# Performance work log

Hardware: AMD Instinct MI355X
Metric: run time of the kernel (lower is better)

The kernel has to match this reference:

```python
import jax, jax.numpy as jnp
import numpy as np
import math

B, L, D, H = 2, 4096, 1024, 16
DH = D // H


def _build_table(seq_len):
    # Faithful port of build_hierarchical_index_lookup_table (static, host-side).
    assert seq_len & (seq_len - 1) == 0
    levels = int(math.log2(seq_len))
    max_valid = 2 * seq_len - 3
    idx = np.full((seq_len, levels), -1, dtype=np.int64)
    cm = np.zeros((seq_len, levels), dtype=bool)
    for n in range(seq_len):
        c = n
        for lvl in range(levels):
            if lvl == 0:
                nxt = c ^ 1
                pair = c
            else:
                nxt = (c // 2 + seq_len) ^ 1
                pair = c // 2 + seq_len
            if nxt > max_valid:
                break
            if pair < nxt:
                cm[n, lvl] = True
            idx[n, lvl] = nxt
            c = nxt
    return idx, cm


def setup_inputs() -> dict:
    rng = jax.random.key(0)
    ks = jax.random.split(rng, 8)
    s = 0.02  # init scale for weights
    idx, cm = _build_table(L)
    return {
        "query": jax.random.normal(ks[0], (B, L, D), jnp.float32),
        "key": jax.random.normal(ks[1], (B, L, D), jnp.float32),
        "value": jax.random.normal(ks[2], (B, L, D), jnp.float32),
        "Wq": jax.random.normal(ks[3], (D, D), jnp.float32) * s,
        "Wk": jax.random.normal(ks[4], (D, D), jnp.float32) * s,
        "Wv": jax.random.normal(ks[5], (D, D), jnp.float32) * s,
        "Wo": jax.random.normal(ks[6], (D, D), jnp.float32) * s,
        "bo": jax.random.normal(ks[7], (D,), jnp.float32) * s,
        "idx_table": jnp.asarray(idx),        # [L, log2(L)] int64
        "causal_mask": jnp.asarray(cm),       # [L, log2(L)] bool
    }


def reference(query, key, value, Wq, Wk, Wv, Wo, bo, idx_table, causal_mask):
    Bq, Lq, Dm = query.shape
    scale = 1.0 / math.sqrt(DH)

    def heads(x, W):  # nn.Linear (no bias) + split heads -> [B,H,L,Dh]
        return (x @ W.T).reshape(Bq, Lq, H, DH).transpose(0, 2, 1, 3)

    Q = heads(query, Wq)
    K = heads(key, Wk)
    V = heads(value, Wv)

    # Build binary-tree hierarchy. Pair weights come from softmax of ZERO
    # logits (Q_parent starts as zeros in the source), so w0 = w1 = 0.5 exactly.
    Ks, Vs = [K], [V]
    while Ks[-1].shape[2] > 1:
        k, v = Ks[-1], Vs[-1]
        Lc = k.shape[2]
        k2 = k.reshape(Bq, H, Lc // 2, 2, DH)
        v2 = v.reshape(Bq, H, Lc // 2, 2, DH)
        Ks.append(0.5 * (k2[:, :, :, 0] + k2[:, :, :, 1]))
        Vs.append(v2[:, :, :, 0] + v2[:, :, :, 1])
    flatK = jnp.concatenate(Ks, axis=2)  # [B,H,2L-1,Dh]
    flatV = jnp.concatenate(Vs, axis=2)

    # Gather neighbor nodes across levels: [B,H,L,levels,Dh]
    nk = flatK[:, :, idx_table]
    nv = flatV[:, :, idx_table]

    self_logits = jnp.einsum('bhnd,bhnd->bhn', Q, K) * scale
    nbr_logits = jnp.einsum('bhld,bhlnd->bhln', Q, nk) * scale
    nbr_logits = jnp.where(causal_mask[None, None], -jnp.inf, nbr_logits)

    all_logits = jnp.concatenate([self_logits[..., None], nbr_logits], axis=-1)
    w = jax.nn.softmax(all_logits, axis=-1)           # [B,H,L,1+levels]
    all_v = jnp.concatenate([V[:, :, :, None, :], nv], axis=3)
    out = jnp.einsum('bhln,bhlnd->bhld', w, all_v)    # [B,H,L,Dh]
    out = out.transpose(0, 2, 1, 3).reshape(Bq, Lq, Dm)
    return out @ Wo.T + bo
```

## Files before the change

kernel.cpp:

```cpp
#include <hip/hip_runtime.h>
#include <cstdint>
#include <cstddef>


typedef __bf16 bf16;
typedef __bf16 bf16x8 __attribute__((ext_vector_type(8)));
typedef __bf16 bf16x4 __attribute__((ext_vector_type(4)));
typedef float  f32x4  __attribute__((ext_vector_type(4)));

#define L_SEQ  4096
#define NFLAT  8192

__device__ __forceinline__ int off_l(int l) { return 8192 - (8192 >> l); }

__device__ __forceinline__ void glds16(const bf16* g, bf16* l) {
  __builtin_amdgcn_global_load_lds(
      (const __attribute__((address_space(1))) unsigned int*)g,
      (__attribute__((address_space(3))) unsigned int*)l, 16, 0, 0);
}

#define MEMFENCE asm volatile("" ::: "memory")
__device__ __forceinline__ void barrier_raw() {
  MEMFENCE; __builtin_amdgcn_s_barrier(); MEMFENCE;
}

__device__ __forceinline__ int swz(int b) { return b ^ (((b >> 9) & 1) << 5); }
__device__ __forceinline__ int la(int row, int col) {
  return ((((row >> 4) << 1) + (col >> 5)) << 10) + ((row & 15) << 6) + ((col & 31) << 1);
}

__global__ __launch_bounds__(256) void cvtall_kernel(
    const float* __restrict__ q, const float* __restrict__ k, const float* __restrict__ v,
    const float* __restrict__ wq, const float* __restrict__ wk,
    const float* __restrict__ wv, const float* __restrict__ wo,
    bf16* __restrict__ qx, bf16* __restrict__ kx, bf16* __restrict__ vx,
    bf16* __restrict__ wqx, bf16* __restrict__ wkx, bf16* __restrict__ wvx,
    bf16* __restrict__ wox) {
  const int y = blockIdx.y;
  int i = blockIdx.x * 256 + threadIdx.x;
  const float* src; bf16* dst;
  if (y < 3) {
    src = (y == 0) ? q : (y == 1) ? k : v;
    dst = (y == 0) ? qx : (y == 1) ? kx : vx;
  } else {
    if (i >= 1048576) return;
    const int w = i >> 18; i &= 262143;
    src = (w == 0) ? wq : (w == 1) ? wk : (w == 2) ? wv : wo;
    dst = (w == 0) ? wqx : (w == 1) ? wkx : (w == 2) ? wvx : wox;
  }
  const float4 t = ((const float4*)src)[i];
  bf16x4 o;
  o[0] = (bf16)t.x; o[1] = (bf16)t.y; o[2] = (bf16)t.z; o[3] = (bf16)t.w;
  *(bf16x4*)(dst + (size_t)i * 4) = o;
}

#define BUFB 32768

__device__ __forceinline__ void stage_tile(const bf16* __restrict__ A,
                                           const bf16* __restrict__ W,
                                           int tm, int tn, int k0,
                                           char* buf, int tid, int wid) {
  bf16* Ad = (bf16*)buf;
  bf16* Bd = (bf16*)(buf + 16384);
#pragma unroll
  for (int i = 0; i < 4; i++) {
    const int d  = i * 4096 + tid * 16;
    const int lb = swz(d);
    const int row = ((lb >> 10) >> 1) * 16 + ((lb >> 6) & 15);
    const int col = ((lb >> 10) & 1) * 32 + ((lb & 63) >> 1);
    glds16(A + (size_t)(tm * 128 + row) * 1024 + k0 + col, Ad + ((i * 4096 + wid * 1024) >> 1));
    glds16(W + (size_t)(tn * 128 + row) * 1024 + k0 + col, Bd + ((i * 4096 + wid * 1024) >> 1));
  }
}

__device__ __forceinline__ void gemm8_core(const bf16* __restrict__ A,
                                           const bf16* __restrict__ W,
                                           int tm, int tn, char* lds,
                                           f32x4 (&acc)[4][4]) {
  const int tid  = threadIdx.x;
  const int wid  = tid >> 6, lane = tid & 63;
  const int wm   = wid >> 1, wn = wid & 1;
  const int laneR  = lane & 15;
  const int laneC8 = (lane >> 4) * 8;

  stage_tile(A, W, tm, tn, 0, lds, tid, wid);

  for (int u = 0; u < 16; ++u) {
    asm volatile("s_waitcnt vmcnt(0)" ::: "memory");
    barrier_raw();
    if (u + 1 < 16)
      stage_tile(A, W, tm, tn, (u + 1) << 6, lds + ((u + 1) & 1) * BUFB, tid, wid);

    const char* Ab = lds + (u & 1) * BUFB;
    const char* Bb = Ab + 16384;
    bf16x8 af[4][2], bfr[4][2];
#pragma unroll
    for (int f = 0; f < 4; f++)
#pragma unroll
      for (int ks = 0; ks < 2; ks++)
        af[f][ks] = *(const bf16x8*)(Ab + swz(la(wm * 64 + f * 16 + laneR, ks * 32 + laneC8)));
#pragma unroll
    for (int j = 0; j < 4; j++)
#pragma unroll
      for (int ks = 0; ks < 2; ks++)
        bfr[j][ks] = *(const bf16x8*)(Bb + swz(la(wn * 64 + j * 16 + laneR, ks * 32 + laneC8)));

    __builtin_amdgcn_s_setprio(1);
#pragma unroll
    for (int f = 0; f < 4; f++)
#pragma unroll
      for (int j = 0; j < 4; j++)
#pragma unroll
        for (int ks = 0; ks < 2; ks++)
          acc[f][j] = __builtin_amdgcn_mfma_f32_16x16x32_bf16(
              af[f][ks], bfr[j][ks], acc[f][j], 0, 0, 0);
    __builtin_amdgcn_s_setprio(0);
  }
}

__device__ __forceinline__ void tile_map(int bid, int& tm, int& tn) {
  const int xcd = bid & 7, q = bid >> 3;
  tm = xcd * 8 + (q >> 3);
  tn = q & 7;
}

__global__ __launch_bounds__(256, 2) void gemm8_qkv_kernel(
    const bf16* __restrict__ qx, const bf16* __restrict__ kx, const bf16* __restrict__ vx,
    const bf16* __restrict__ wq, const bf16* __restrict__ wk, const bf16* __restrict__ wv,
    bf16* __restrict__ Qb, bf16* __restrict__ fK, bf16* __restrict__ fV) {
  __shared__ __align__(16) char lds[2 * BUFB];
  const int z = blockIdx.y;
  const bf16* A = (z == 0) ? qx : (z == 1) ? kx : vx;
  const bf16* W = (z == 0) ? wq : (z == 1) ? wk : wv;
  bf16* D       = (z == 0) ? Qb : (z == 1) ? fK : fV;
  const int lstr = (z == 0) ? L_SEQ : NFLAT;
  int tm, tn; tile_map(blockIdx.x, tm, tn);
  f32x4 acc[4][4] = {};
  gemm8_core(A, W, tm, tn, lds, acc);

  const int lane = threadIdx.x & 63, wid = threadIdx.x >> 6;
  const int rl0 = (wid >> 1) * 64 + (lane >> 4) * 4;
  const int cl0 = (wid & 1) * 64 + (lane & 15);
#pragma unroll
  for (int i = 0; i < 4; i++)
#pragma unroll
    for (int j = 0; j < 4; j++)
#pragma unroll
      for (int r = 0; r < 4; r++) {
        const int m = tm * 128 + rl0 + i * 16 + r;
        const int n = tn * 128 + cl0 + j * 16;
        const int b = m >> 12, l = m & 4095;
        const int h = n >> 6,  dh = n & 63;
        D[((size_t)(b * 16 + h) * lstr + l) * 64 + dh] = (bf16)acc[i][j][r];
      }

  if (z != 0) {
    bf16* Ct = (bf16*)lds;
    barrier_raw();
#pragma unroll
    for (int i = 0; i < 4; i++)
#pragma unroll
      for (int j = 0; j < 4; j++)
#pragma unroll
        for (int r = 0; r < 4; r++)
          Ct[(rl0 + i * 16 + r) * 132 + (cl0 + j * 16)] = (bf16)acc[i][j][r];
    barrier_raw();

    const int g2 = threadIdx.x >> 7;
    const int c  = threadIdx.x & 127;
    const int h  = tn * 2 + (c >> 6), dh = c & 63;
    const int b  = (tm * 128) >> 12;
    const int lbase = ((tm * 128) & 4095) + g2 * 64;
    const size_t fb = (size_t)(b * 16 + h) * NFLAT * 64 + dh;
    float pk[7];
#pragma unroll
    for (int i = 0; i < 64; i++) {
      float ck = (float)Ct[(g2 * 64 + i) * 132 + c];
#pragma unroll
      for (int l = 1; l <= 6; l++) {
        if (((i + 1) & ((1 << l) - 1)) != 0) { pk[l] = ck; break; }
        ck += pk[l];
        const int j = (lbase + i) >> l;
        D[fb + (size_t)(off_l(l) + j) * 64] =
            (bf16)(z == 1 ? ck * (1.0f / (1 << l)) : ck);
      }
    }
  }
}

__global__ __launch_bounds__(256, 2) void gemm8_out_kernel(
    const bf16* __restrict__ Ob, const bf16* __restrict__ wo,
    const float* __restrict__ bo, float* __restrict__ out) {
  __shared__ __align__(16) char lds[2 * BUFB];
  int tm, tn; tile_map(blockIdx.x, tm, tn);
  f32x4 acc[4][4] = {};
  gemm8_core(Ob, wo, tm, tn, lds, acc);
  const int lane = threadIdx.x & 63, wid = threadIdx.x >> 6;
  const int m0 = tm * 128 + (wid >> 1) * 64 + (lane >> 4) * 4;
  const int n0 = tn * 128 + (wid & 1) * 64 + (lane & 15);
#pragma unroll
  for (int i = 0; i < 4; i++)
#pragma unroll
    for (int j = 0; j < 4; j++)
#pragma unroll
      for (int r = 0; r < 4; r++) {
        const int m = m0 + i * 16 + r;
        const int n = n0 + j * 16;
        out[(size_t)m * 1024 + n] = acc[i][j][r] + bo[n];
      }
}

__global__ __launch_bounds__(64) void tree_l712(bf16* __restrict__ fK, bf16* __restrict__ fV) {
  __shared__ float Ks[64 * 64];
  __shared__ float Vs[64 * 64];
  const int bh = blockIdx.x, d = threadIdx.x;
  const size_t fb = (size_t)bh * NFLAT * 64;
#pragma unroll 8
  for (int i = 0; i < 64; i++) {
    Ks[i * 64 + d] = (float)fK[fb + (size_t)(8064 + i) * 64 + d];
    Vs[i * 64 + d] = (float)fV[fb + (size_t)(8064 + i) * 64 + d];
  }
#pragma unroll
  for (int l = 7; l <= 12; l++) {
    const int cnt = 4096 >> l;
    for (int j = 0; j < cnt; j++) {
      const float k = (Ks[(2 * j) * 64 + d] + Ks[(2 * j + 1) * 64 + d]) * 0.5f;
      const float v =  Vs[(2 * j) * 64 + d] + Vs[(2 * j + 1) * 64 + d];
      Ks[j * 64 + d] = k;
      Vs[j * 64 + d] = v;
      fK[fb + (size_t)(off_l(l) + j) * 64 + d] = (bf16)k;
      fV[fb + (size_t)(off_l(l) + j) * 64 + d] = (bf16)v;
    }
  }
}

__global__ __launch_bounds__(64) void attn_kernel(
    const bf16* __restrict__ Qb, const bf16* __restrict__ fK,
    const bf16* __restrict__ fV, bf16* __restrict__ Ob) {
  __shared__ __align__(16) unsigned short Kl[132 * 64];
  __shared__ __align__(16) unsigned short Vl[132 * 64];
  const int t0  = blockIdx.x * 64;
  const int bh  = blockIdx.y;
  const int tid = threadIdx.x;
  const size_t fb = (size_t)bh * NFLAT * 64;

  for (int u = tid; u < 132 * 8; u += 64) {
    const int r = u >> 3, c = u & 7;
    int flat;
    if      (r < 64)  flat = t0 + r;
    else if (r < 96)  flat = 4096 + (t0 >> 1) + (r - 64);
    else if (r < 112) flat = 6144 + (t0 >> 2) + (r - 96);
    else if (r < 120) flat = 7168 + (t0 >> 3) + (r - 112);
    else if (r < 124) flat = 7680 + (t0 >> 4) + (r - 120);
    else if (r < 126) flat = 7936 + (t0 >> 5) + (r - 124);
    else { const int l = r - 120; flat = (8192 - (8192 >> l) + (t0 >> l)) ^ 1; }
    const int cc = c ^ (r & 7);
    const uint4 kk = *(const uint4*)((const char*)(fK + fb + (size_t)flat * 64) + c * 16);
    const uint4 vv = *(const uint4*)((const char*)(fV + fb + (size_t)flat * 64) + c * 16);
    *(uint4*)((char*)Kl + r * 128 + cc * 16) = kk;
    *(uint4*)((char*)Vl + r * 128 + cc * 16) = vv;
  }
  __syncthreads();

  const int n = t0 + tid;
  int rows[13];
  rows[0] = tid;
#pragma unroll
  for (int l = 0; l < 12; l++) {
    int r;
    if (l == 0)      r = tid ^ 1;
    else if (l <= 5) r = (128 - (128 >> l)) + (((n >> l) ^ 1) - (t0 >> l));
    else             r = 126 + (l - 6);
    rows[l + 1] = r;
  }

  float q[64];
  const bf16* Qr = Qb + ((size_t)bh * L_SEQ + n) * 64;
#pragma unroll
  for (int c = 0; c < 8; c++) {
    bf16x8 v = *(const bf16x8*)(Qr + c * 8);
#pragma unroll
    for (int j = 0; j < 8; j++) q[c * 8 + j] = (float)v[j];
  }

  float lg[13];
#pragma unroll
  for (int v = 0; v < 13; v++) {
    const int r = rows[v];
    float a = 0.f;
#pragma unroll
    for (int c = 0; c < 8; c++) {
      const int cc = c ^ (r & 7);
      const bf16x8 kv = *(const bf16x8*)((const char*)Kl + r * 128 + cc * 16);
#pragma unroll
      for (int j = 0; j < 8; j++) a += q[c * 8 + j] * (float)kv[j];
    }
    lg[v] = a * 0.125f;
  }
#pragma unroll
  for (int v = 1; v < 13; v++)
    if (!((n >> (v - 1)) & 1)) lg[v] = -1e30f;

  float mx = lg[0];
#pragma unroll
  for (int v = 1; v < 13; v++) mx = fmaxf(mx, lg[v]);
  float w[13], s = 0.f;
#pragma unroll
  for (int v = 0; v < 13; v++) { w[v] = __expf(lg[v] - mx); s += w[v]; }
  const float inv = 1.0f / s;

  float o[64];
#pragma unroll
  for (int d = 0; d < 64; d++) o[d] = 0.f;
#pragma unroll
  for (int v = 0; v < 13; v++) {
    const int r = rows[v];
    const float wv = w[v];
#pragma unroll
    for (int c = 0; c < 8; c++) {
      const int cc = c ^ (r & 7);
      const bf16x8 vv = *(const bf16x8*)((const char*)Vl + r * 128 + cc * 16);
#pragma unroll
      for (int j = 0; j < 8; j++) o[c * 8 + j] += wv * (float)vv[j];
    }
  }

  bf16* Or = Ob + ((size_t)(bh >> 4) * L_SEQ + n) * 1024 + (size_t)(bh & 15) * 64;
#pragma unroll
  for (int c = 0; c < 8; c++) {
    bf16x8 ov;
#pragma unroll
    for (int j = 0; j < 8; j++) ov[j] = (bf16)(o[c * 8 + j] * inv);
    *(bf16x8*)(Or + c * 8) = ov;
  }
}

extern "C" void kernel_launch(void* const* d_in, const int* in_sizes, int n_in,
                              void* d_out, int out_size, void* d_ws, size_t ws_size,
                              hipStream_t stream) {
  const float* query = (const float*)d_in[0];
  const float* key   = (const float*)d_in[1];
  const float* value = (const float*)d_in[2];
  const float* Wq    = (const float*)d_in[3];
  const float* Wk    = (const float*)d_in[4];
  const float* Wv    = (const float*)d_in[5];
  const float* Wo    = (const float*)d_in[6];
  const float* bo    = (const float*)d_in[7];
  float* out = (float*)d_out;

  char* ws = (char*)d_ws;
  size_t off = 0;
  auto take = [&](size_t bytes) -> void* {
    void* p = ws + off;
    off += (bytes + 255) & ~(size_t)255;
    return p;
  };
  const size_t XB = (size_t)8192 * 1024 * 2;
  const size_t WB = (size_t)1024 * 1024 * 2;
  bf16* qx  = (bf16*)take(XB);
  bf16* kx  = (bf16*)take(XB);
  bf16* vx  = (bf16*)take(XB);
  bf16* wqx = (bf16*)take(WB);
  bf16* wkx = (bf16*)take(WB);
  bf16* wvx = (bf16*)take(WB);
  bf16* wox = (bf16*)take(WB);
  bf16* Qb  = (bf16*)take((size_t)32 * L_SEQ * 64 * 2);
  bf16* fK  = (bf16*)take((size_t)32 * NFLAT * 64 * 2);
  bf16* fV  = (bf16*)take((size_t)32 * NFLAT * 64 * 2);
  bf16* Ob  = qx;
  (void)in_sizes; (void)n_in; (void)out_size; (void)ws_size;

  cvtall_kernel<<<dim3(8192, 4), 256, 0, stream>>>(
      query, key, value, Wq, Wk, Wv, Wo, qx, kx, vx, wqx, wkx, wvx, wox);

  gemm8_qkv_kernel<<<dim3(512, 3), 256, 0, stream>>>(qx, kx, vx, wqx, wkx, wvx, Qb, fK, fV);

  tree_l712<<<32, 64, 0, stream>>>(fK, fV);

  attn_kernel<<<dim3(64, 32), 64, 0, stream>>>(Qb, fK, fV, Ob);

  gemm8_out_kernel<<<512, 256, 0, stream>>>(Ob, wox, bo, out);
}
```

Baseline: 160.9 us.

## Use grid-stride 8-wide conversion and read level-0 K/V directly from global in attention

The fp32-to-bf16 conversion kernel becomes a grid-stride loop over a fixed 2048-block grid, with each thread converting eight elements (two float4 loads, one 16-byte store) instead of four. The attention kernel no longer stages the 64 level-0 K/V rows in shared memory. Each thread reads its own row and its sibling's row straight from global memory, which shrinks LDS use from 132 to 68 rows per tensor. This aims to cut launch and staging overhead and raise occupancy, at the cost of uncoalesced per-thread global reads for the self and sibling rows.

```diff
diff --git a/kernel.cpp b/kernel.cpp
--- a/kernel.cpp
+++ b/kernel.cpp
@@ -36,22 +36,26 @@
     bf16* __restrict__ qx, bf16* __restrict__ kx, bf16* __restrict__ vx,
     bf16* __restrict__ wqx, bf16* __restrict__ wkx, bf16* __restrict__ wvx,
     bf16* __restrict__ wox) {
-  const int y = blockIdx.y;
-  int i = blockIdx.x * 256 + threadIdx.x;
-  const float* src; bf16* dst;
-  if (y < 3) {
-    src = (y == 0) ? q : (y == 1) ? k : v;
-    dst = (y == 0) ? qx : (y == 1) ? kx : vx;
-  } else {
-    if (i >= 1048576) return;
-    const int w = i >> 18; i &= 262143;
-    src = (w == 0) ? wq : (w == 1) ? wk : (w == 2) ? wv : wo;
-    dst = (w == 0) ? wqx : (w == 1) ? wkx : (w == 2) ? wvx : wox;
-  }
-  const float4 t = ((const float4*)src)[i];
-  bf16x4 o;
-  o[0] = (bf16)t.x; o[1] = (bf16)t.y; o[2] = (bf16)t.z; o[3] = (bf16)t.w;
-  *(bf16x4*)(dst + (size_t)i * 4) = o;
+  for (int i = blockIdx.x * 256 + threadIdx.x; i < 3670016; i += 524288) {
+    int g = i;
+    const float* s; bf16* d;
+    if (g < 3145728) {
+      const int t = g >> 20; g &= 1048575;
+      s = (t == 0) ? q : (t == 1) ? k : v;
+      d = (t == 0) ? qx : (t == 1) ? kx : vx;
+    } else {
+      int gg = g - 3145728;
+      const int t = gg >> 17; g = gg & 131071;
+      s = (t == 0) ? wq : (t == 1) ? wk : (t == 2) ? wv : wo;
+      d = (t == 0) ? wqx : (t == 1) ? wkx : (t == 2) ? wvx : wox;
+    }
+    const float4 v0 = ((const float4*)s)[(size_t)g * 2];
+    const float4 v1 = ((const float4*)s)[(size_t)g * 2 + 1];
+    bf16x8 o;
+    o[0] = (bf16)v0.x; o[1] = (bf16)v0.y; o[2] = (bf16)v0.z; o[3] = (bf16)v0.w;
+    o[4] = (bf16)v1.x; o[5] = (bf16)v1.y; o[6] = (bf16)v1.z; o[7] = (bf16)v1.w;
+    *(bf16x8*)(d + (size_t)g * 8) = o;
+  }
 }
 
 #define BUFB 32768
@@ -237,23 +241,22 @@
 __global__ __launch_bounds__(64) void attn_kernel(
     const bf16* __restrict__ Qb, const bf16* __restrict__ fK,
     const bf16* __restrict__ fV, bf16* __restrict__ Ob) {
-  __shared__ __align__(16) unsigned short Kl[132 * 64];
-  __shared__ __align__(16) unsigned short Vl[132 * 64];
+  __shared__ __align__(16) unsigned short Kl[68 * 64];
+  __shared__ __align__(16) unsigned short Vl[68 * 64];
   const int t0  = blockIdx.x * 64;
   const int bh  = blockIdx.y;
   const int tid = threadIdx.x;
   const size_t fb = (size_t)bh * NFLAT * 64;
 
-  for (int u = tid; u < 132 * 8; u += 64) {
+  for (int u = tid; u < 68 * 8; u += 64) {
     const int r = u >> 3, c = u & 7;
     int flat;
-    if      (r < 64)  flat = t0 + r;
-    else if (r < 96)  flat = 4096 + (t0 >> 1) + (r - 64);
-    else if (r < 112) flat = 6144 + (t0 >> 2) + (r - 96);
-    else if (r < 120) flat = 7168 + (t0 >> 3) + (r - 112);
-    else if (r < 124) flat = 7680 + (t0 >> 4) + (r - 120);
-    else if (r < 126) flat = 7936 + (t0 >> 5) + (r - 124);
-    else { const int l = r - 120; flat = (8192 - (8192 >> l) + (t0 >> l)) ^ 1; }
+    if      (r < 32) flat = 4096 + (t0 >> 1) + r;
+    else if (r < 48) flat = 6144 + (t0 >> 2) + (r - 32);
+    else if (r < 56) flat = 7168 + (t0 >> 3) + (r - 48);
+    else if (r < 60) flat = 7680 + (t0 >> 4) + (r - 56);
+    else if (r < 62) flat = 7936 + (t0 >> 5) + (r - 60);
+    else { const int l = r - 56; flat = (8192 - (8192 >> l) + (t0 >> l)) ^ 1; }
     const int cc = c ^ (r & 7);
     const uint4 kk = *(const uint4*)((const char*)(fK + fb + (size_t)flat * 64) + c * 16);
     const uint4 vv = *(const uint4*)((const char*)(fV + fb + (size_t)flat * 64) + c * 16);
@@ -264,13 +267,11 @@
 
   const int n = t0 + tid;
   int rows[13];
-  rows[0] = tid;
-#pragma unroll
-  for (int l = 0; l < 12; l++) {
+#pragma unroll
+  for (int l = 1; l < 12; l++) {
     int r;
-    if (l == 0)      r = tid ^ 1;
-    else if (l <= 5) r = (128 - (128 >> l)) + (((n >> l) ^ 1) - (t0 >> l));
-    else             r = 126 + (l - 6);
+    if (l <= 5) r = (64 - (128 >> l)) + (((n >> l) ^ 1) - (t0 >> l));
+    else        r = 62 + (l - 6);
     rows[l + 1] = r;
   }
 
@@ -284,8 +285,21 @@
   }
 
   float lg[13];
-#pragma unroll
-  for (int v = 0; v < 13; v++) {
+  {
+    const bf16* Ks0 = fK + fb + (size_t)(t0 + tid) * 64;
+    const bf16* Kn0 = fK + fb + (size_t)(t0 + (tid ^ 1)) * 64;
+    float a0 = 0.f, a1 = 0.f;
+#pragma unroll
+    for (int c = 0; c < 8; c++) {
+      const bf16x8 s = *(const bf16x8*)(Ks0 + c * 8);
+      const bf16x8 t = *(const bf16x8*)(Kn0 + c * 8);
+#pragma unroll
+      for (int j = 0; j < 8; j++) { a0 += q[c * 8 + j] * (float)s[j]; a1 += q[c * 8 + j] * (float)t[j]; }
+    }
+    lg[0] = a0 * 0.125f; lg[1] = a1 * 0.125f;
+  }
+#pragma unroll
+  for (int v = 2; v < 13; v++) {
     const int r = rows[v];
     float a = 0.f;
 #pragma unroll
@@ -312,8 +326,20 @@
   float o[64];
 #pragma unroll
   for (int d = 0; d < 64; d++) o[d] = 0.f;
-#pragma unroll
-  for (int v = 0; v < 13; v++) {
+  {
+    const bf16* Vs0 = fV + fb + (size_t)(t0 + tid) * 64;
+    const bf16* Vn0 = fV + fb + (size_t)(t0 + (tid ^ 1)) * 64;
+    const float w0 = w[0], w1 = w[1];
+#pragma unroll
+    for (int c = 0; c < 8; c++) {
+      const bf16x8 s0 = *(const bf16x8*)(Vs0 + c * 8);
+      const bf16x8 t1 = *(const bf16x8*)(Vn0 + c * 8);
+#pragma unroll
+      for (int j = 0; j < 8; j++) o[c * 8 + j] += w0 * (float)s0[j] + w1 * (float)t1[j];
+    }
+  }
+#pragma unroll
+  for (int v = 2; v < 13; v++) {
     const int r = rows[v];
     const float wv = w[v];
 #pragma unroll
@@ -370,7 +396,7 @@
   bf16* Ob  = qx;
   (void)in_sizes; (void)n_in; (void)out_size; (void)ws_size;
 
-  cvtall_kernel<<<dim3(8192, 4), 256, 0, stream>>>(
+  cvtall_kernel<<<2048, 256, 0, stream>>>(
       query, key, value, Wq, Wk, Wv, Wo, qx, kx, vx, wqx, wkx, wvx, wox);
 
   gemm8_qkv_kernel<<<dim3(512, 3), 256, 0, stream>>>(qx, kx, vx, wqx, wkx, wvx, Qb, fK, fV);
```

New measurement: 159.5 us. No clear change (-0.9%).
